# Kernel optimization log

Measured on AMD Instinct MI355X. Metric: run time of the kernel, lower is better.

The kernel has to match this reference:

```python
import jax, jax.numpy as jnp
import numpy as np

NUM_BITS = 4
N_VAL = 2 ** NUM_BITS - 1            # 15
INTERVAL = 2.0 / N_VAL               # init_range / n_val (non-trainable)
ZERO = 0.0                           # self.zero (non-trainable, default init)
EPS = 1e-3


def setup_inputs() -> dict:
    key = jax.random.key(0)
    k1, k2 = jax.random.split(key)
    x = jax.random.normal(k1, (32, 256, 56, 56), dtype=jnp.float32)
    # learned bin widths, initialized near `interval` with some spread
    a = (INTERVAL * (0.8 + 0.4 * jax.random.uniform(k2, (N_VAL,)))).astype(jnp.float32)
    start = jnp.full((1,), -1.0, dtype=jnp.float32)  # quantization range start
    scale1 = jnp.ones((1,), dtype=jnp.float32)
    scale2 = jnp.ones((1,), dtype=jnp.float32)
    return {"x": x, "start": start, "a": a, "scale1": scale1, "scale2": scale2}


def reference(x, start, a, scale1, scale2):
    xs = x * scale1                              # broadcast scalar
    s = start[0]
    a_pos = jnp.where(a > EPS, a, EPS)           # [n_val]
    cums = jnp.cumsum(a_pos)                     # [n_val]
    # thre_backward[i] = start + sum_{j<i} a_pos[j]
    tb = s + jnp.concatenate([jnp.zeros((1,), a_pos.dtype), cums[:-1]])
    # thre_forward[i] = thre_backward[i] + a_pos[i]/2
    tf = tb + a_pos * 0.5
    dt = xs.dtype

    # forward (hard) branch: count of strict exceedances of the sorted tf
    cnt_f = jnp.searchsorted(tf, xs, side="left")        # in [0, n_val]
    x_forward = ZERO + cnt_f.astype(dt) * jnp.asarray(INTERVAL, dt)

    # backward (soft) branch: piecewise-linear interpolation within the active bin
    cnt_b = jnp.searchsorted(tb, xs, side="left")        # in [0, n_val]
    idx = jnp.clip(cnt_b - 1, 0, N_VAL - 1)
    lin = (INTERVAL / a_pos[idx]) * (xs - tb[idx]) + ZERO + idx.astype(dt) * INTERVAL
    x_backward = jnp.where(cnt_b == 0, jnp.asarray(ZERO, dt), lin)
    top = s + cums[-1]                                    # last thre_backward + a_pos[-1]
    x_backward = jnp.where(xs > top, jnp.asarray(2.0, dt), x_backward)

    # straight-through combine: value from x_forward, gradient from x_backward
    out = jax.lax.stop_gradient(x_forward) + x_backward - jax.lax.stop_gradient(x_backward)
    return out * scale2
```

## Files before the change

### kernel.cpp

```cpp
#include <hip/hip_runtime.h>

#define NVAL 15
#define TPB  256
#define VPT  8

typedef float fvec4 __attribute__((ext_vector_type(4)));

__device__ __forceinline__ void make_thresholds(
    const float* __restrict__ start, const float* __restrict__ a,
    const float* __restrict__ scale1, const float* __restrict__ scale2,
    float* tf, float& sc1, float& k)
{
    const float s = start[0];
    sc1 = scale1[0];
    k   = (float)(2.0 / 15.0) * scale2[0];
    float cum = 0.0f;
#pragma unroll
    for (int i = 0; i < NVAL; ++i) {
        float ai = a[i];
        float ap = (ai > 1e-3f) ? ai : 1e-3f;
        tf[i] = (s + cum) + 0.5f * ap;
        cum += ap;
    }
}

__device__ __forceinline__ fvec4 quant4(fvec4 v, const float* tf, float sc1, float k)
{
    float xs0 = v.x * sc1, xs1 = v.y * sc1, xs2 = v.z * sc1, xs3 = v.w * sc1;
    int c0 = 0, c1 = 0, c2 = 0, c3 = 0;
#pragma unroll
    for (int i = 0; i < NVAL; ++i) {
        float t = tf[i];
        c0 += (xs0 > t);
        c1 += (xs1 > t);
        c2 += (xs2 > t);
        c3 += (xs3 > t);
    }
    fvec4 r;
    r.x = k * (float)c0;
    r.y = k * (float)c1;
    r.z = k * (float)c2;
    r.w = k * (float)c3;
    return r;
}

__global__ __launch_bounds__(TPB) void ltq_main(
    const float* __restrict__ x,
    const float* __restrict__ start,
    const float* __restrict__ a,
    const float* __restrict__ scale1,
    const float* __restrict__ scale2,
    float* __restrict__ out)
{
    float tf[NVAL], sc1, k;
    make_thresholds(start, a, scale1, scale2, tf, sc1, k);

    const long long base = (long long)blockIdx.x * (TPB * VPT) + threadIdx.x;
    const fvec4* __restrict__ x4 = (const fvec4*)x + base;
    fvec4* __restrict__ o4 = (fvec4*)out + base;

    fvec4 v[VPT];
#pragma unroll
    for (int j = 0; j < VPT; ++j) v[j] = x4[j * TPB];

#pragma unroll
    for (int j = 0; j < VPT; ++j) {
        fvec4 r = quant4(v[j], tf, sc1, k);
        __builtin_nontemporal_store(r, &o4[j * TPB]);
    }
}

__global__ __launch_bounds__(TPB) void ltq_tail(
    const float* __restrict__ x,
    const float* __restrict__ start,
    const float* __restrict__ a,
    const float* __restrict__ scale1,
    const float* __restrict__ scale2,
    float* __restrict__ out,
    long long f4_done, long long n4, long long n)
{
    float tf[NVAL], sc1, k;
    make_thresholds(start, a, scale1, scale2, tf, sc1, k);

    const long long stride = (long long)gridDim.x * blockDim.x;
    const fvec4* __restrict__ x4 = (const fvec4*)x;
    fvec4* __restrict__ o4 = (fvec4*)out;
    for (long long i = f4_done + blockIdx.x * (long long)blockDim.x + threadIdx.x;
         i < n4; i += stride) {
        fvec4 r = quant4(x4[i], tf, sc1, k);
        __builtin_nontemporal_store(r, &o4[i]);
    }
    for (long long i = (n4 << 2) + blockIdx.x * (long long)blockDim.x + threadIdx.x;
         i < n; i += stride) {
        float xs = x[i] * sc1;
        int c = 0;
#pragma unroll
        for (int t = 0; t < NVAL; ++t) c += (xs > tf[t]);
        out[i] = k * (float)c;
    }
}

extern "C" void kernel_launch(void* const* d_in, const int* in_sizes, int n_in,
                              void* d_out, int out_size, void* d_ws, size_t ws_size,
                              hipStream_t stream) {
    const float* x      = (const float*)d_in[0];
    const float* start  = (const float*)d_in[1];
    const float* a      = (const float*)d_in[2];
    const float* scale1 = (const float*)d_in[3];
    const float* scale2 = (const float*)d_in[4];
    float* out = (float*)d_out;

    const long long n  = in_sizes[0];
    const long long n4 = n >> 2;
    const long long per_block = (long long)TPB * VPT;
    const long long blocks = n4 / per_block;

    if (blocks > 0) {
        ltq_main<<<(int)blocks, TPB, 0, stream>>>(x, start, a, scale1, scale2, out);
    }
    const long long f4_done = blocks * per_block;
    if (f4_done < n4 || (n & 3)) {
        ltq_tail<<<512, TPB, 0, stream>>>(x, start, a, scale1, scale2, out,
                                          f4_done, n4, n);
    }
}
```

Measured before the change: 189.6 us.

## Stage input through LDS via global_load_lds DMA and halve per-block work

Replaces direct register loads with __builtin_amdgcn_global_load_lds 16-byte transfers into a 16KB shared buffer, then reads it back from LDS after a barrier. Block work drops from 2048 to 1024 float4s, so twice as many blocks launch. Nontemporal stores become regular stores. The aim is to free VGPRs and let the DMA path overlap loads with the threshold setup, at the cost of an LDS round trip, a block-wide barrier, and losing the streaming-store hint on a write-once output.

```diff
diff --git a/kernel.cpp b/kernel.cpp
--- a/kernel.cpp
+++ b/kernel.cpp
@@ -2,9 +2,17 @@
 
 #define NVAL 15
 #define TPB  256
-#define VPT  8
+#define F4_PER_BLOCK 1024
+#define F4_PER_THREAD 4
 
 typedef float fvec4 __attribute__((ext_vector_type(4)));
+
+__device__ __forceinline__ void gl2lds16(const float* g, void* lds_uniform_base) {
+    __builtin_amdgcn_global_load_lds(
+        (const __attribute__((address_space(1))) void*)g,
+        (__attribute__((address_space(3))) void*)lds_uniform_base,
+        16, 0, 0);
+}
 
 __device__ __forceinline__ void make_thresholds(
     const float* __restrict__ start, const float* __restrict__ a,
@@ -44,7 +52,7 @@
     return r;
 }
 
-__global__ __launch_bounds__(TPB) void ltq_main(
+__global__ __launch_bounds__(TPB) void ltq_dma(
     const float* __restrict__ x,
     const float* __restrict__ start,
     const float* __restrict__ a,
@@ -52,21 +60,32 @@
     const float* __restrict__ scale2,
     float* __restrict__ out)
 {
+    __shared__ float smem[F4_PER_BLOCK * 4];
+
+    const int wave = threadIdx.x >> 6;
+    const int lane = threadIdx.x & 63;
+    const long long base4 = (long long)blockIdx.x * F4_PER_BLOCK;
+    const float* gbase = x + (base4 << 2);
+
+#pragma unroll
+    for (int j = 0; j < 4; ++j) {
+        const int off_b = (wave * 4 + j) * 1024;
+        gl2lds16(gbase + (off_b >> 2) + lane * 4,
+                 (char*)smem + off_b);
+    }
+
     float tf[NVAL], sc1, k;
     make_thresholds(start, a, scale1, scale2, tf, sc1, k);
 
-    const long long base = (long long)blockIdx.x * (TPB * VPT) + threadIdx.x;
-    const fvec4* __restrict__ x4 = (const fvec4*)x + base;
-    fvec4* __restrict__ o4 = (fvec4*)out + base;
+    __syncthreads();
 
-    fvec4 v[VPT];
+    fvec4* __restrict__ o4 = (fvec4*)out + base4;
+    const fvec4* __restrict__ l4 = (const fvec4*)smem;
 #pragma unroll
-    for (int j = 0; j < VPT; ++j) v[j] = x4[j * TPB];
-
-#pragma unroll
-    for (int j = 0; j < VPT; ++j) {
-        fvec4 r = quant4(v[j], tf, sc1, k);
-        __builtin_nontemporal_store(r, &o4[j * TPB]);
+    for (int j = 0; j < F4_PER_THREAD; ++j) {
+        fvec4 v = l4[threadIdx.x + j * TPB];
+        fvec4 r = quant4(v, tf, sc1, k);
+        o4[threadIdx.x + j * TPB] = r;
     }
 }
 
@@ -87,8 +106,7 @@
     fvec4* __restrict__ o4 = (fvec4*)out;
     for (long long i = f4_done + blockIdx.x * (long long)blockDim.x + threadIdx.x;
          i < n4; i += stride) {
-        fvec4 r = quant4(x4[i], tf, sc1, k);
-        __builtin_nontemporal_store(r, &o4[i]);
+        o4[i] = quant4(x4[i], tf, sc1, k);
     }
     for (long long i = (n4 << 2) + blockIdx.x * (long long)blockDim.x + threadIdx.x;
          i < n; i += stride) {
@@ -112,13 +130,12 @@
 
     const long long n  = in_sizes[0];
     const long long n4 = n >> 2;
-    const long long per_block = (long long)TPB * VPT;
-    const long long blocks = n4 / per_block;
+    const long long blocks = n4 / F4_PER_BLOCK;
 
     if (blocks > 0) {
-        ltq_main<<<(int)blocks, TPB, 0, stream>>>(x, start, a, scale1, scale2, out);
+        ltq_dma<<<(int)blocks, TPB, 0, stream>>>(x, start, a, scale1, scale2, out);
     }
-    const long long f4_done = blocks * per_block;
+    const long long f4_done = blocks * F4_PER_BLOCK;
     if (f4_done < n4 || (n & 3)) {
         ltq_tail<<<512, TPB, 0, stream>>>(x, start, a, scale1, scale2, out,
                                           f4_done, n4, n);
```

Measured after the change: 187.6 us. About the same (-1.1%).
